# Kernel optimization log

Hardware: AMD Instinct MI355X
Metric: run time of the kernel (lower is better)

## Reference

```python
import jax, jax.numpy as jnp
import numpy as np

B, C, H, W = 16, 4, 512, 512
ALPHA, BETA, GAMMA = 1.0, 0.7, 2.0
UPPER, LOWER = 1000.0, 200.0
W_UPPER, W_LOWER = 2.5, 20.0
SMOOTH = 1.0


def setup_inputs() -> dict:
    key = jax.random.key(0)
    k1, k2, k3 = jax.random.split(key, 3)
    outputs = jax.random.normal(k1, (B, C, H, W), dtype=jnp.float32)
    class_weight = jax.random.uniform(k2, (C,), dtype=jnp.float32, minval=0.5, maxval=2.0)
    targets = jax.random.randint(k3, (B, H, W), 0, C, dtype=jnp.int32)
    return {"outputs": outputs, "class_weight": class_weight, "targets": targets}


def _cc_dynamic_weights(tgt):
    """4-connected components of (tgt==2), then per-region area-based weight.

    tgt: [H, W] int32. Returns [H, W] float32 dynamic weight (1.0 off-mask).
    Equivalent to scipy.ndimage.label (default 4-connectivity) + per-region
    piecewise-linear weight, done GPU-side via min-label propagation with
    pointer jumping.
    """
    BIG = H * W  # sentinel label for background
    mask = tgt == 2
    idx = jnp.arange(BIG, dtype=jnp.int32).reshape(H, W)
    lbl0 = jnp.where(mask, idx, BIG)

    def cond(state):
        prev, cur = state
        return jnp.any(prev != cur)

    def body(state):
        _, lbl = state
        p = jnp.pad(lbl, 1, constant_values=BIG)
        nmin = jnp.minimum(jnp.minimum(p[:-2, 1:-1], p[2:, 1:-1]),
                           jnp.minimum(p[1:-1, :-2], p[1:-1, 2:]))
        new = jnp.where(mask, jnp.minimum(lbl, nmin), BIG)
        # pointer jumping: label <- label of my current label's pixel
        new = jnp.where(mask, new.reshape(-1)[new], BIG)  # OOB gather clipped, then masked
        return (lbl, new)

    _, lbl = jax.lax.while_loop(cond, body, (jnp.full_like(lbl0, -1), lbl0))

    # region area per pixel via scatter-add on root labels (background -> bin BIG)
    counts = jnp.zeros(BIG + 1, jnp.float32).at[lbl.reshape(-1)].add(
        mask.reshape(-1).astype(jnp.float32))
    area = counts[lbl]  # [H, W]

    interp = W_UPPER + (W_LOWER - W_UPPER) * (UPPER - area) / (UPPER - LOWER)
    rw = jnp.where(area > UPPER, W_UPPER, jnp.where(area < LOWER, W_LOWER, interp))
    return jnp.where(mask, rw, 1.0).astype(jnp.float32)


def reference(outputs, class_weight, targets):
    nc = outputs.shape[1]
    # weighted per-pixel cross entropy (reduction='none')
    logp = jax.nn.log_softmax(outputs, axis=1)  # [B,C,H,W]
    nll = -jnp.take_along_axis(logp, targets[:, None, :, :], axis=1)[:, 0]  # [B,H,W]
    ce = class_weight[targets] * nll  # [B,H,W]

    dyn = jax.vmap(_cc_dynamic_weights)(targets)  # [B,H,W]
    weighted_ce = jnp.mean(ce * dyn)

    probs = jax.nn.softmax(outputs, axis=1)
    one_hot = jax.nn.one_hot(targets, nc, dtype=jnp.float32).transpose(0, 3, 1, 2)
    inter = jnp.sum(probs * one_hot, axis=(2, 3))  # [B,C]
    dice = (2.0 * inter + SMOOTH) / (jnp.sum(probs, axis=(2, 3)) + jnp.sum(one_hot, axis=(2, 3)) + SMOOTH)
    dice_loss = 1.0 - jnp.mean(dice)

    pt = jnp.exp(-ce)
    focal = jnp.mean(ALPHA * (1.0 - pt) ** GAMMA * ce)

    return BETA * weighted_ce + (1.0 - BETA) * dice_loss + focal
```

## Files before the change

kernel.cpp:

```cpp
#include <hip/hip_runtime.h>


namespace {
constexpr int IMG_W = 512;
constexpr int NB    = 16;
constexpr int NC    = 4;
constexpr int HW    = 512 * 512;
constexpr int NPIX  = NB * HW;
constexpr int SLAB  = 4096;
constexpr int NSLAB = NPIX / SLAB;
constexpr int NID   = NPIX / 2;
constexpr int LOSS_BLOCKS = 2048;
constexpr int PART_STRIDE = 16;
constexpr float ALPHA  = 1.0f;
constexpr float BETA   = 0.7f;
constexpr float UPPER  = 1000.0f;
constexpr float LOWER  = 200.0f;
constexpr float W_UP   = 2.5f;
constexpr float W_LO   = 20.0f;
constexpr float SMOOTH = 1.0f;
}

__device__ __forceinline__ int ld_par(const int* parent, int i) {
    return __hip_atomic_load(&parent[i], __ATOMIC_RELAXED, __HIP_MEMORY_SCOPE_AGENT);
}

__device__ __forceinline__ int find_root_atomic(int* parent, int x) {
    int p = ld_par(parent, x);
    while (p != x) { x = p; p = ld_par(parent, x); }
    return x;
}

__device__ __forceinline__ void unite(int* parent, int a, int b) {
    int ra = find_root_atomic(parent, a);
    int rb = find_root_atomic(parent, b);
    while (ra != rb) {
        int lo = ra < rb ? ra : rb;
        int hi = ra < rb ? rb : ra;
        int old = atomicCAS(&parent[hi], hi, lo);
        if (old == hi) return;
        ra = find_root_atomic(parent, old);
        rb = find_root_atomic(parent, lo);
    }
}

__device__ __forceinline__ float wave_reduce(float v) {
    #pragma unroll
    for (int off = 32; off > 0; off >>= 1) v += __shfl_down(v, off);
    return v;
}

__global__ void __launch_bounds__(256)
k1_init(const int* __restrict__ tgt, int* parent) {
    const int tid = threadIdx.x, bid = blockIdx.x;
    const int base = bid * SLAB;
    const int lane = tid & 63;

    unsigned mk16 = 0;
    #pragma unroll
    for (int it = 0; it < 16; ++it) {
        int px = base + it * 256 + tid;
        bool mk = (tgt[px] == 2);
        mk16 |= (unsigned)mk << it;
        unsigned long long bal = __ballot(mk);
        int par = -1;
        if (mk) {
            unsigned long long below = (1ull << lane) - 1ull;
            unsigned long long zb = (~bal) & below;
            int rs = (zb == 0ull) ? 0 : (64 - __clzll(zb));
            par = px - lane + rs;
        }
        parent[px] = par;
    }
    __syncthreads();
    #pragma unroll 1
    for (int it = 0; it < 16; ++it) {
        if (!((mk16 >> it) & 1u)) continue;
        int px = base + it * 256 + tid;
        if (lane == 0 && (px & (IMG_W - 1)) != 0 && tgt[px - 1] == 2)
            unite(parent, px, px - 1);
        if (it >= 2 && ((mk16 >> (it - 2)) & 1u))
            unite(parent, px, px - IMG_W);
    }
}

__global__ void __launch_bounds__(256)
k2_boundary(const int* __restrict__ tgt, int* parent, int* __restrict__ counts) {
    int gid = blockIdx.x * 256 + threadIdx.x;
    *reinterpret_cast<int4*>(&counts[gid * 4]) = make_int4(0, 0, 0, 0);
    int s   = gid >> 9;
    int col = gid & 511;
    if ((s & 63) == 0) return;
    int px = s * SLAB + col;
    if (tgt[px] == 2 && tgt[px - IMG_W] == 2) unite(parent, px, px - IMG_W);
}

__global__ void __launch_bounds__(256)
k3_flatten(int* parent, int* counts) {
    int q0 = (blockIdx.x * 256 + threadIdx.x) * 4;
    int4 pv = *reinterpret_cast<const int4*>(&parent[q0]);
    int vj[4] = {pv.x, pv.y, pv.z, pv.w};
    bool any = false;
    #pragma unroll
    for (int j = 0; j < 4; ++j) {
        int v = vj[j];
        if (v == -1) continue;
        int id;
        while (true) {
            if (v <= -2) { id = -2 - v; break; }
            int nxt = ld_par(parent, v);
            if (nxt == v)  { id = v >> 1; break; }
            if (nxt <= -2) { id = -2 - nxt; break; }
            v = nxt;
        }
        vj[j] = -2 - id;
        any = true;
        atomicAdd(&counts[id], 1);
    }
    if (any)
        *reinterpret_cast<int4*>(&parent[q0]) = make_int4(vj[0], vj[1], vj[2], vj[3]);
}

__global__ void __launch_bounds__(256)
k4_loss(const float* __restrict__ logits, const float* __restrict__ cw,
        const int* __restrict__ tgt, const int* __restrict__ parent,
        const int* __restrict__ counts, float* __restrict__ partials) {
    const int bid = blockIdx.x, tid = threadIdx.x;
    const int b    = bid >> 7;
    const int slab = bid & 127;
    const float* Lb = logits + (size_t)b * NC * HW;
    const int*   Tb = tgt + (size_t)b * HW;
    const int*   Pb = parent + (size_t)b * HW;
    float cw0 = cw[0], cw1 = cw[1], cw2 = cw[2], cw3 = cw[3];

    float a_wce = 0.f, a_foc = 0.f;
    float a_ps[4] = {0.f, 0.f, 0.f, 0.f};
    float a_in[4] = {0.f, 0.f, 0.f, 0.f};
    float a_ct[4] = {0.f, 0.f, 0.f, 0.f};

    #pragma unroll
    for (int it = 0; it < 2; ++it) {
        int p = slab * 2048 + (it * 256 + tid) * 4;
        int4 t4 = *reinterpret_cast<const int4*>(&Tb[p]);
        int4 e4 = *reinterpret_cast<const int4*>(&Pb[p]);
        int tj[4] = {t4.x, t4.y, t4.z, t4.w};
        int ej[4] = {e4.x, e4.y, e4.z, e4.w};
        float4 x0 = *reinterpret_cast<const float4*>(&Lb[p]);
        float4 x1 = *reinterpret_cast<const float4*>(&Lb[p + HW]);
        float4 x2 = *reinterpret_cast<const float4*>(&Lb[p + 2 * HW]);
        float4 x3 = *reinterpret_cast<const float4*>(&Lb[p + 3 * HW]);
        float c0[4] = {x0.x, x0.y, x0.z, x0.w};
        float c1[4] = {x1.x, x1.y, x1.z, x1.w};
        float c2[4] = {x2.x, x2.y, x2.z, x2.w};
        float c3[4] = {x3.x, x3.y, x3.z, x3.w};
        #pragma unroll
        for (int j = 0; j < 4; ++j) {
            float v0 = c0[j], v1 = c1[j], v2 = c2[j], v3 = c3[j];
            int   t  = tj[j];
            float m  = fmaxf(fmaxf(v0, v1), fmaxf(v2, v3));
            float e0 = __expf(v0 - m), e1 = __expf(v1 - m);
            float e2 = __expf(v2 - m), e3 = __expf(v3 - m);
            float S  = e0 + e1 + e2 + e3;
            float invS = __frcp_rn(S);
            float xt = (t == 0) ? v0 : (t == 1) ? v1 : (t == 2) ? v2 : v3;
            float wt = (t == 0) ? cw0 : (t == 1) ? cw1 : (t == 2) ? cw2 : cw3;
            float nll = __logf(S) + m - xt;
            float ce  = wt * nll;
            float pt  = __expf(-ce);
            float omp = 1.0f - pt;
            float focal_i = ALPHA * omp * omp * ce;
            float dyn = 1.0f;
            if (t == 2) {
                float area = (float)counts[-2 - ej[j]];
                float interp = W_UP + (W_LO - W_UP) * (UPPER - area) * (1.0f / (UPPER - LOWER));
                dyn = (area > UPPER) ? W_UP : (area < LOWER) ? W_LO : interp;
            }
            float pr0 = e0 * invS, pr1 = e1 * invS, pr2 = e2 * invS, pr3 = e3 * invS;
            float prt = (t == 0) ? pr0 : (t == 1) ? pr1 : (t == 2) ? pr2 : pr3;
            a_wce += ce * dyn;
            a_foc += focal_i;
            a_ps[0] += pr0; a_ps[1] += pr1; a_ps[2] += pr2; a_ps[3] += pr3;
            a_in[t] += prt;
            a_ct[t] += 1.0f;
        }
    }

    float vals[14];
    vals[0] = a_wce; vals[1] = a_foc;
    vals[2] = a_ps[0]; vals[3] = a_ps[1]; vals[4] = a_ps[2]; vals[5] = a_ps[3];
    vals[6] = a_in[0]; vals[7] = a_in[1]; vals[8] = a_in[2]; vals[9] = a_in[3];
    vals[10] = a_ct[0]; vals[11] = a_ct[1]; vals[12] = a_ct[2]; vals[13] = a_ct[3];

    __shared__ float red[14][4];
    int lane = tid & 63, wv = tid >> 6;
    #pragma unroll
    for (int i = 0; i < 14; ++i) {
        float v = wave_reduce(vals[i]);
        if (lane == 0) red[i][wv] = v;
    }
    __syncthreads();
    if (tid < 14)
        partials[bid * PART_STRIDE + tid] =
            red[tid][0] + red[tid][1] + red[tid][2] + red[tid][3];
}

__global__ void __launch_bounds__(1024)
k5_final(const float* __restrict__ partials, float* __restrict__ out) {
    int tid = threadIdx.x, lane = tid & 63, w = tid >> 6;
    const float* r0 = &partials[(w * 128 + lane) * PART_STRIDE];
    const float* r1 = &partials[(w * 128 + 64 + lane) * PART_STRIDE];
    float v[14];
    #pragma unroll
    for (int i = 0; i < 14; ++i) v[i] = r0[i] + r1[i];
    #pragma unroll
    for (int i = 0; i < 14; ++i) v[i] = wave_reduce(v[i]);

    __shared__ double s_wce[16], s_foc[16], s_dice[16];
    if (lane == 0) {
        double dsum = 0.0;
        #pragma unroll
        for (int c = 0; c < 4; ++c) {
            double inter = v[6 + c], psum = v[2 + c], cnt = v[10 + c];
            dsum += (2.0 * inter + (double)SMOOTH) / (psum + cnt + (double)SMOOTH);
        }
        s_wce[w] = v[0]; s_foc[w] = v[1]; s_dice[w] = dsum;
    }
    __syncthreads();
    if (tid == 0) {
        double wce = 0.0, foc = 0.0, dice = 0.0;
        for (int i = 0; i < 16; ++i) { wce += s_wce[i]; foc += s_foc[i]; dice += s_dice[i]; }
        double dice_mean = dice / (double)(NB * NC);
        out[0] = (float)((double)BETA * (wce / (double)NPIX)
                         + (1.0 - (double)BETA) * (1.0 - dice_mean)
                         + (foc / (double)NPIX));
    }
}

extern "C" void kernel_launch(void* const* d_in, const int* in_sizes, int n_in,
                              void* d_out, int out_size, void* d_ws, size_t ws_size,
                              hipStream_t stream) {
    const float* logits = (const float*)d_in[0];
    const float* cw     = (const float*)d_in[1];
    const int*   tgt    = (const int*)d_in[2];
    float*       out    = (float*)d_out;
    char*        ws     = (char*)d_ws;
    int*   parent   = (int*)ws;
    int*   counts   = (int*)(ws + (size_t)NPIX * 4);
    float* partials = (float*)(ws + (size_t)NPIX * 4 + (size_t)NID * 4);

    hipLaunchKernelGGL(k1_init, dim3(NSLAB), dim3(256), 0, stream, tgt, parent);
    hipLaunchKernelGGL(k2_boundary, dim3(NID / 4 / 256), dim3(256), 0, stream,
                       tgt, parent, counts);
    hipLaunchKernelGGL(k3_flatten, dim3(NPIX / 1024), dim3(256), 0, stream,
                       parent, counts);
    hipLaunchKernelGGL(k4_loss, dim3(LOSS_BLOCKS), dim3(256), 0, stream,
                       logits, cw, tgt, parent, counts, partials);
    hipLaunchKernelGGL(k5_final, dim3(1), dim3(1024), 0, stream, partials, out);
}
```

Baseline: 203.7 us.

## Do slab-local union-find in LDS and flatten to roots before global merge

```diff
diff --git a/kernel.cpp b/kernel.cpp
--- a/kernel.cpp
+++ b/kernel.cpp
@@ -25,22 +25,45 @@
     return __hip_atomic_load(&parent[i], __ATOMIC_RELAXED, __HIP_MEMORY_SCOPE_AGENT);
 }
 
-__device__ __forceinline__ int find_root_atomic(int* parent, int x) {
+__device__ __forceinline__ int find_root_g(int* parent, int x) {
     int p = ld_par(parent, x);
     while (p != x) { x = p; p = ld_par(parent, x); }
     return x;
 }
 
-__device__ __forceinline__ void unite(int* parent, int a, int b) {
-    int ra = find_root_atomic(parent, a);
-    int rb = find_root_atomic(parent, b);
+__device__ __forceinline__ void unite_g(int* parent, int a, int b) {
+    int ra = find_root_g(parent, a);
+    int rb = find_root_g(parent, b);
     while (ra != rb) {
         int lo = ra < rb ? ra : rb;
         int hi = ra < rb ? rb : ra;
         int old = atomicCAS(&parent[hi], hi, lo);
         if (old == hi) return;
-        ra = find_root_atomic(parent, old);
-        rb = find_root_atomic(parent, lo);
+        ra = find_root_g(parent, old);
+        rb = find_root_g(parent, lo);
+    }
+}
+
+__device__ __forceinline__ int ld_lp(int* lp, int i) {
+    return __hip_atomic_load(&lp[i], __ATOMIC_RELAXED, __HIP_MEMORY_SCOPE_WORKGROUP);
+}
+
+__device__ __forceinline__ int find_l(int* lp, int x) {
+    int p = ld_lp(lp, x);
+    while (p != x) { x = p; p = ld_lp(lp, x); }
+    return x;
+}
+
+__device__ __forceinline__ void unite_l(int* lp, int a, int b) {
+    int ra = find_l(lp, a);
+    int rb = find_l(lp, b);
+    while (ra != rb) {
+        int lo = ra < rb ? ra : rb;
+        int hi = ra < rb ? rb : ra;
+        int old = atomicCAS(&lp[hi], hi, lo);
+        if (old == hi) return;
+        ra = find_l(lp, old);
+        rb = find_l(lp, lo);
     }
 }
 
@@ -51,7 +74,9 @@
 }
 
 __global__ void __launch_bounds__(256)
-k1_init(const int* __restrict__ tgt, int* parent) {
+k1_init(const int* __restrict__ tgt, int* __restrict__ parent,
+        int* __restrict__ counts) {
+    __shared__ int lp[SLAB];
     const int tid = threadIdx.x, bid = blockIdx.x;
     const int base = bid * SLAB;
     const int lane = tid & 63;
@@ -59,8 +84,8 @@
     unsigned mk16 = 0;
     #pragma unroll
     for (int it = 0; it < 16; ++it) {
-        int px = base + it * 256 + tid;
-        bool mk = (tgt[px] == 2);
+        int l = it * 256 + tid;
+        bool mk = (tgt[base + l] == 2);
         mk16 |= (unsigned)mk << it;
         unsigned long long bal = __ballot(mk);
         int par = -1;
@@ -68,31 +93,53 @@
             unsigned long long below = (1ull << lane) - 1ull;
             unsigned long long zb = (~bal) & below;
             int rs = (zb == 0ull) ? 0 : (64 - __clzll(zb));
-            par = px - lane + rs;
-        }
-        parent[px] = par;
+            par = l - lane + rs;
+        }
+        lp[l] = par;
+    }
+    {
+        int c0 = bid * (NID / NSLAB) + tid * 8;
+        *reinterpret_cast<int4*>(&counts[c0])     = make_int4(0, 0, 0, 0);
+        *reinterpret_cast<int4*>(&counts[c0 + 4]) = make_int4(0, 0, 0, 0);
     }
     __syncthreads();
+
     #pragma unroll 1
     for (int it = 0; it < 16; ++it) {
         if (!((mk16 >> it) & 1u)) continue;
-        int px = base + it * 256 + tid;
-        if (lane == 0 && (px & (IMG_W - 1)) != 0 && tgt[px - 1] == 2)
-            unite(parent, px, px - 1);
+        int l = it * 256 + tid;
+        if (lane == 0 && (l & (IMG_W - 1)) != 0 && ld_lp(lp, l - 1) >= 0)
+            unite_l(lp, l, l - 1);
         if (it >= 2 && ((mk16 >> (it - 2)) & 1u))
-            unite(parent, px, px - IMG_W);
+            unite_l(lp, l, l - IMG_W);
+    }
+    __syncthreads();
+
+    #pragma unroll
+    for (int q = 0; q < 4; ++q) {
+        int l0 = (q * 256 + tid) * 4;
+        int vj[4];
+        #pragma unroll
+        for (int j = 0; j < 4; ++j) {
+            int l = l0 + j;
+            int p = lp[l];
+            if (p < 0) { vj[j] = -1; continue; }
+            while (true) { int n = lp[p]; if (n == p) break; p = n; }
+            vj[j] = base + p;
+        }
+        *reinterpret_cast<int4*>(&parent[base + l0]) =
+            make_int4(vj[0], vj[1], vj[2], vj[3]);
     }
 }
 
 __global__ void __launch_bounds__(256)
-k2_boundary(const int* __restrict__ tgt, int* parent, int* __restrict__ counts) {
+k2_boundary(const int* __restrict__ tgt, int* parent) {
     int gid = blockIdx.x * 256 + threadIdx.x;
-    *reinterpret_cast<int4*>(&counts[gid * 4]) = make_int4(0, 0, 0, 0);
     int s   = gid >> 9;
     int col = gid & 511;
     if ((s & 63) == 0) return;
     int px = s * SLAB + col;
-    if (tgt[px] == 2 && tgt[px - IMG_W] == 2) unite(parent, px, px - IMG_W);
+    if (tgt[px] == 2 && tgt[px - IMG_W] == 2) unite_g(parent, px, px - IMG_W);
 }
 
 __global__ void __launch_bounds__(256)
@@ -248,9 +295,10 @@
     int*   counts   = (int*)(ws + (size_t)NPIX * 4);
     float* partials = (float*)(ws + (size_t)NPIX * 4 + (size_t)NID * 4);
 
-    hipLaunchKernelGGL(k1_init, dim3(NSLAB), dim3(256), 0, stream, tgt, parent);
-    hipLaunchKernelGGL(k2_boundary, dim3(NID / 4 / 256), dim3(256), 0, stream,
+    hipLaunchKernelGGL(k1_init, dim3(NSLAB), dim3(256), 0, stream,
                        tgt, parent, counts);
+    hipLaunchKernelGGL(k2_boundary, dim3(NSLAB * IMG_W / 256), dim3(256), 0, stream,
+                       tgt, parent);
     hipLaunchKernelGGL(k3_flatten, dim3(NPIX / 1024), dim3(256), 0, stream,
                        parent, counts);
     hipLaunchKernelGGL(k4_loss, dim3(LOSS_BLOCKS), dim3(256), 0, stream,
```

Result: faster. 183.5 us (-9.9%).
